# Kernel optimization log

Measured on AMD Instinct MI355X. Metric: run time of the kernel, lower is better.

## Reference

```python
import jax, jax.numpy as jnp
import numpy as np

H = 12
D_MODEL = 768
H_D = D_MODEL // H


def setup_inputs() -> dict:
    key = jax.random.key(0)
    ks = jax.random.split(key, 11)
    B, S = 2, 2048
    scale_in = 1.0
    w_scale = 1.0 / np.sqrt(D_MODEL)
    inp = {
        "query": jax.random.normal(ks[0], (B, S, D_MODEL), dtype=jnp.float32),
        "key": jax.random.normal(ks[1], (B, S, D_MODEL), dtype=jnp.float32),
        "value": jax.random.normal(ks[2], (B, S, D_MODEL), dtype=jnp.float32),
        "wq": jax.random.normal(ks[3], (D_MODEL, D_MODEL), dtype=jnp.float32) * w_scale,
        "bq": jnp.zeros((D_MODEL,), dtype=jnp.float32),
        "wk": jax.random.normal(ks[4], (D_MODEL, D_MODEL), dtype=jnp.float32) * w_scale,
        "bk": jnp.zeros((D_MODEL,), dtype=jnp.float32),
        "wv": jax.random.normal(ks[5], (D_MODEL, D_MODEL), dtype=jnp.float32) * w_scale,
        "bv": jnp.zeros((D_MODEL,), dtype=jnp.float32),
        "wo": jax.random.normal(ks[6], (D_MODEL, D_MODEL), dtype=jnp.float32) * w_scale,
        "bo": jnp.zeros((D_MODEL,), dtype=jnp.float32),
    }
    return inp


def reference(query, key, value, wq, bq, wk, bk, wv, bv, wo, bo):
    B, S, _ = query.shape
    # QKV projections, split into heads: [B, H, S, h_d]
    def proj(x, w, b):
        y = jnp.einsum("bsd,de->bse", x, w) + b
        return y.reshape(B, S, H, H_D).transpose(0, 2, 1, 3)

    q = proj(query, wq, bq)
    k = proj(key, wk, bk)
    v = proj(value, wv, bv)

    # scaled dot-product attention (dropout disabled / eval mode)
    scores = jnp.einsum("bhsd,bhtd->bhst", q, k) / jnp.sqrt(jnp.float32(H_D))
    wm = jax.nn.softmax(scores, axis=-1)  # [B, H, S, S]
    out = jnp.einsum("bhst,bhtd->bhsd", wm, v)

    # merge heads and output projection
    out = out.transpose(0, 2, 1, 3).reshape(B, S, D_MODEL)
    out = jnp.einsum("bsd,de->bse", out, wo) + bo
    return out
```

## Files before the change

kernel.cpp:

```cpp
#include <hip/hip_runtime.h>

#define H 12
#define DM 768
#define HD 64
#define SEQ 2048
#define BATCH 2
#define MROWS (BATCH*SEQ)

typedef __attribute__((ext_vector_type(8))) short short8;
typedef __attribute__((ext_vector_type(4))) float f32x4;
using u16 = unsigned short;
using u32 = unsigned int;

__device__ __forceinline__ float bf2f(u16 u) { return __uint_as_float(((u32)u) << 16); }
__device__ __forceinline__ u16 f2bf(float x) {
  u32 u = __float_as_uint(x);
  return (u16)((u + 0x7fffu + ((u >> 16) & 1u)) >> 16);
}
__device__ __forceinline__ u32 cvt_pk_bf16(float lo, float hi) {
  u32 r;
  asm("v_cvt_pk_bf16_f32 %0, %1, %2" : "=v"(r) : "v"(lo), "v"(hi));
  return r;
}
__device__ __forceinline__ void gl2lds16(const u16* __restrict__ g, u16* l) {
  __builtin_amdgcn_global_load_lds(
      (const __attribute__((address_space(1))) unsigned int*)g,
      (__attribute__((address_space(3))) unsigned int*)l,
      16, 0, 0);
}

#define C_SM 0.18033688011112042f

__global__ __launch_bounds__(256) void transpose_w4(const float* __restrict__ w0, const float* __restrict__ w1,
                                                    const float* __restrict__ w2, const float* __restrict__ w3,
                                                    u16* __restrict__ dst0)
{
  __shared__ u16 Ts[64][72];
  const float* src = blockIdx.z == 0 ? w0 : blockIdx.z == 1 ? w1 : blockIdx.z == 2 ? w2 : w3;
  u16* dst = dst0 + (size_t)blockIdx.z * DM * DM;
  const int t = threadIdx.x;
  const int r0 = blockIdx.y * 64, c0 = blockIdx.x * 64;
  const int row = t >> 2, cq = (t & 3) * 16;
  const float* sp = src + (size_t)(r0 + row) * DM + c0 + cq;
  #pragma unroll
  for (int g = 0; g < 4; ++g) {
    float4 a = *reinterpret_cast<const float4*>(sp + g * 4);
    Ts[row][cq + g * 4 + 0] = f2bf(a.x);
    Ts[row][cq + g * 4 + 1] = f2bf(a.y);
    Ts[row][cq + g * 4 + 2] = f2bf(a.z);
    Ts[row][cq + g * 4 + 3] = f2bf(a.w);
  }
  __syncthreads();
  union { uint4 v[2]; u16 e[16]; } pk;
  #pragma unroll
  for (int j = 0; j < 16; ++j) pk.e[j] = Ts[cq + j][row];
  uint4* dp = reinterpret_cast<uint4*>(dst + (size_t)(c0 + row) * DM + r0 + cq);
  dp[0] = pk.v[0];
  dp[1] = pk.v[1];
}

template<int BM, bool AF32>
__device__ __forceinline__ void gemm_core(const void* __restrict__ Av, const u16* __restrict__ Bt,
                                          const float* __restrict__ bias, void* __restrict__ dstv,
                                          int mode, int bx, int by, float outScale)
{
  constexpr int AFR = BM / 32;
  constexpr int ACH = BM / 32;
  __shared__ u16 As[BM * 64];
  __shared__ u16 Bs[128 * 64];
  const int t = threadIdx.x;
  const int lane = t & 63, w = t >> 6;
  const int l15 = lane & 15, l4 = lane >> 4;
  const int m0 = by * BM, n0 = bx * 128;
  const int wr = (w >> 1) * (BM / 2), wc = (w & 1) * 64;

  f32x4 acc[AFR][4] = {};

  for (int kt = 0; kt < DM / 64; ++kt) {
    const int k0 = kt * 64;
    #pragma unroll
    for (int c = 0; c < ACH; ++c) {
      const int id = c * 256 + t;
      const int row = id >> 3, xc = id & 7;
      const int db = row * 128 + ((xc * 16) ^ ((row & 7) << 4));
      if (AF32) {
        const float* Af = reinterpret_cast<const float*>(Av) + (size_t)(m0 + row) * DM + k0 + xc * 8;
        float4 a0 = *reinterpret_cast<const float4*>(Af);
        float4 a1 = *reinterpret_cast<const float4*>(Af + 4);
        uint4 v;
        v.x = cvt_pk_bf16(a0.x, a0.y);
        v.y = cvt_pk_bf16(a0.z, a0.w);
        v.z = cvt_pk_bf16(a1.x, a1.y);
        v.w = cvt_pk_bf16(a1.z, a1.w);
        *reinterpret_cast<uint4*>(reinterpret_cast<char*>(As) + db) = v;
      } else {
        uint4 va = *reinterpret_cast<const uint4*>(reinterpret_cast<const u16*>(Av) +
                   (size_t)(m0 + row) * DM + k0 + xc * 8);
        *reinterpret_cast<uint4*>(reinterpret_cast<char*>(As) + db) = va;
      }
    }
    #pragma unroll
    for (int c = 0; c < 4; ++c) {
      const int id = c * 256 + t;
      const int row = id >> 3, xc = id & 7;
      const int db = row * 128 + ((xc * 16) ^ ((row & 7) << 4));
      uint4 vb = *reinterpret_cast<const uint4*>(Bt + (size_t)(n0 + row) * DM + k0 + xc * 8);
      *reinterpret_cast<uint4*>(reinterpret_cast<char*>(Bs) + db) = vb;
    }
    __syncthreads();
    #pragma unroll
    for (int ks = 0; ks < 2; ++ks) {
      short8 ag[AFR], bg[4];
      #pragma unroll
      for (int i = 0; i < AFR; ++i) {
        const int ar = wr + i * 16 + l15;
        ag[i] = *reinterpret_cast<const short8*>(reinterpret_cast<const char*>(As) +
                 ar * 128 + ((ks * 64 + l4 * 16) ^ ((ar & 7) << 4)));
      }
      #pragma unroll
      for (int j = 0; j < 4; ++j) {
        const int br = wc + j * 16 + l15;
        bg[j] = *reinterpret_cast<const short8*>(reinterpret_cast<const char*>(Bs) +
                 br * 128 + ((ks * 64 + l4 * 16) ^ ((br & 7) << 4)));
      }
      #pragma unroll
      for (int i = 0; i < AFR; ++i)
        #pragma unroll
        for (int j = 0; j < 4; ++j)
          acc[i][j] = __builtin_amdgcn_mfma_f32_16x16x32_bf16(ag[i], bg[j], acc[i][j], 0, 0, 0);
    }
    __syncthreads();
  }

  #pragma unroll
  for (int j = 0; j < 4; ++j) {
    const int gcol = n0 + wc + j * 16 + l15;
    const float bb = bias[gcol];
    #pragma unroll
    for (int i = 0; i < AFR; ++i) {
      const int grow = m0 + wr + i * 16 + l4 * 4;
      if (mode == 2) {
        float* dst = reinterpret_cast<float*>(dstv);
        #pragma unroll
        for (int r = 0; r < 4; ++r)
          dst[(size_t)(grow + r) * DM + gcol] = acc[i][j][r] + bb;
      } else {
        u16* dst = reinterpret_cast<u16*>(dstv);
        const int b = grow >> 11, s = grow & (SEQ - 1);
        const int h = gcol >> 6, d = gcol & 63;
        if (mode == 0) {
          #pragma unroll
          for (int r = 0; r < 4; ++r)
            dst[((size_t)(b * H + h) * SEQ + s + r) * HD + d] = f2bf((acc[i][j][r] + bb) * outScale);
        } else {
          union { uint2 v; u16 e[4]; } pk;
          #pragma unroll
          for (int r = 0; r < 4; ++r) pk.e[r] = f2bf(acc[i][j][r] + bb);
          *reinterpret_cast<uint2*>(dst + ((size_t)(b * H + h) * HD + d) * SEQ + s) = pk.v;
        }
      }
    }
  }
}

__global__ __launch_bounds__(256) void gemm_qkv_kernel(
    const float* __restrict__ xq, const float* __restrict__ xk, const float* __restrict__ xv,
    const u16* __restrict__ wT, const float* __restrict__ bq, const float* __restrict__ bk,
    const float* __restrict__ bv, u16* __restrict__ Qb, u16* __restrict__ Kb, u16* __restrict__ Vtb)
{
  const int flat = blockIdx.z * 384 + blockIdx.y * 6 + blockIdx.x;
  const int nb = (flat & 7) * 144 + (flat >> 3);
  const int z = nb / 384, rem = nb % 384;
  const int by = rem / 6, bx = rem % 6;
  const float* A    = z == 0 ? xq : z == 1 ? xk : xv;
  const u16* Bt     = wT + (size_t)z * DM * DM;
  const float* bias = z == 0 ? bq : z == 1 ? bk : bv;
  u16* dst          = z == 0 ? Qb : z == 1 ? Kb : Vtb;
  const float sc    = z == 1 ? C_SM : 1.0f;
  gemm_core<64, true>(A, Bt, bias, dst, z == 2 ? 1 : 0, bx, by, sc);
}

__global__ __launch_bounds__(256) void gemm_o_kernel(const u16* __restrict__ A, const u16* __restrict__ woT,
                                                     const float* __restrict__ bo, float* __restrict__ out)
{
  const int flat = blockIdx.y * 6 + blockIdx.x;
  const int nb = (flat & 7) * 96 + (flat >> 3);
  gemm_core<32, false>(A, woT, bo, out, 2, nb % 6, nb / 6, 1.0f);
}

__global__ __launch_bounds__(256) void attn_kernel(const u16* __restrict__ Q, const u16* __restrict__ K,
                                                   const u16* __restrict__ Vt, u16* __restrict__ attn)
{
  __shared__ u16 Ks[2][64 * 64];
  __shared__ u16 Vs[2][64 * 64];
  __shared__ u16 Ps[4][16 * 64];
  const int t = threadIdx.x;
  const int lane = t & 63, w = t >> 6;
  const int l15 = lane & 15, l4 = lane >> 4;
  const int flat = blockIdx.y * 32 + blockIdx.x;
  const int nbid = (flat & 7) * 96 + (flat >> 3);
  const int q0 = (nbid & 31) * 64;
  const int bh = nbid >> 5;
  const size_t qbase  = ((size_t)bh * SEQ + q0) * HD;
  const size_t kbase0 = (size_t)bh * SEQ * HD;
  const size_t vtbase = (size_t)bh * HD * SEQ;

  const int srow = lane >> 3;
  const int scol = ((lane & 7) ^ srow) * 8;

  u16* Qstage = &Ps[0][0];
  #pragma unroll
  for (int j = 0; j < 2; ++j) {
    const int ci = w * 2 + j;
    gl2lds16(Q + qbase + (size_t)(ci * 8 + srow) * HD + scol, &Qstage[ci * 512]);
  }
  #pragma unroll
  for (int j = 0; j < 2; ++j) {
    const int ci = w * 2 + j;
    const int row = ci * 8 + srow;
    gl2lds16(K + kbase0 + (size_t)row * HD + scol, &Ks[0][ci * 512]);
    gl2lds16(Vt + vtbase + (size_t)row * SEQ + scol, &Vs[0][ci * 512]);
  }
  asm volatile("s_waitcnt vmcnt(4)" ::: "memory");
  __builtin_amdgcn_s_barrier();

  short8 qf[2];
  {
    const int qr = w * 16 + l15;
    #pragma unroll
    for (int ks = 0; ks < 2; ++ks)
      qf[ks] = *reinterpret_cast<const short8*>(reinterpret_cast<const char*>(Qstage) +
               qr * 128 + ((ks * 64 + l4 * 16) ^ ((qr & 7) << 4)));
  }
  asm volatile("s_waitcnt lgkmcnt(0)" ::: "memory");
  __builtin_amdgcn_s_barrier();

  short8 ones;
  #pragma unroll
  for (int j = 0; j < 8; ++j) ones[j] = (short)0x3F80;

  f32x4 oacc[4] = {};
  f32x4 accL = {};
  char* Pw = reinterpret_cast<char*>(Ps[w]);
  const int pswz = (l15 & 7) << 4;
  int cur = 0;

  for (int kt = 0; kt < SEQ / 64; ++kt) {
    asm volatile("s_waitcnt vmcnt(0)" ::: "memory");
    __builtin_amdgcn_s_barrier();

    if (kt + 1 < SEQ / 64) {
      const int nxt = cur ^ 1;
      #pragma unroll
      for (int j = 0; j < 2; ++j) {
        const int ci = w * 2 + j;
        const int row = ci * 8 + srow;
        gl2lds16(K + kbase0 + (size_t)((kt + 1) * 64 + row) * HD + scol, &Ks[nxt][ci * 512]);
        gl2lds16(Vt + vtbase + (size_t)row * SEQ + (kt + 1) * 64 + scol, &Vs[nxt][ci * 512]);
      }
    }

    f32x4 sacc[4] = {};
    #pragma unroll
    for (int ks = 0; ks < 2; ++ks) {
      #pragma unroll
      for (int kb = 0; kb < 4; ++kb) {
        const int krow = kb * 16 + l15;
        short8 kf = *reinterpret_cast<const short8*>(reinterpret_cast<const char*>(Ks[cur]) +
                    krow * 128 + ((ks * 64 + l4 * 16) ^ ((krow & 7) << 4)));
        sacc[kb] = __builtin_amdgcn_mfma_f32_16x16x32_bf16(kf, qf[ks], sacc[kb], 0, 0, 0);
      }
    }

    #pragma unroll
    for (int kb = 0; kb < 4; ++kb) {
      const float p0 = exp2f(sacc[kb][0]);
      const float p1 = exp2f(sacc[kb][1]);
      const float p2 = exp2f(sacc[kb][2]);
      const float p3 = exp2f(sacc[kb][3]);
      uint2 pk;
      pk.x = cvt_pk_bf16(p0, p1);
      pk.y = cvt_pk_bf16(p2, p3);
      *reinterpret_cast<uint2*>(Pw + (l15 * 128 + ((kb * 32 + l4 * 8) ^ pswz))) = pk;
    }

    #pragma unroll
    for (int ks = 0; ks < 2; ++ks) {
      short8 pf = *reinterpret_cast<const short8*>(Pw +
                  (l15 * 128 + ((ks * 64 + l4 * 16) ^ pswz)));
      accL = __builtin_amdgcn_mfma_f32_16x16x32_bf16(pf, ones, accL, 0, 0, 0);
      #pragma unroll
      for (int nb = 0; nb < 4; ++nb) {
        const int vrow = nb * 16 + l15;
        short8 vf = *reinterpret_cast<const short8*>(reinterpret_cast<const char*>(Vs[cur]) +
                    vrow * 128 + ((ks * 64 + l4 * 16) ^ ((vrow & 7) << 4)));
        oacc[nb] = __builtin_amdgcn_mfma_f32_16x16x32_bf16(pf, vf, oacc[nb], 0, 0, 0);
      }
    }
    cur ^= 1;
  }

  const int b = bh / H, h = bh % H;
  #pragma unroll
  for (int r = 0; r < 4; ++r) {
    const float inv = 1.f / accL[r];
    const int srow2 = q0 + w * 16 + l4 * 4 + r;
    const size_t base = ((size_t)(b * SEQ + srow2)) * DM + h * HD;
    #pragma unroll
    for (int nb = 0; nb < 4; ++nb)
      attn[base + nb * 16 + l15] = f2bf(oacc[nb][r] * inv);
  }
}

extern "C" void kernel_launch(void* const* d_in, const int* in_sizes, int n_in,
                              void* d_out, int out_size, void* d_ws, size_t ws_size,
                              hipStream_t stream)
{
  const float* q  = (const float*)d_in[0];
  const float* k  = (const float*)d_in[1];
  const float* v  = (const float*)d_in[2];
  const float* wq = (const float*)d_in[3];
  const float* bq = (const float*)d_in[4];
  const float* wk = (const float*)d_in[5];
  const float* bk = (const float*)d_in[6];
  const float* wv = (const float*)d_in[7];
  const float* bv = (const float*)d_in[8];
  const float* wo = (const float*)d_in[9];
  const float* bo = (const float*)d_in[10];

  u16* ws = (u16*)d_ws;
  const size_t WSZ = (size_t)DM * DM;
  const size_t TSZ = (size_t)MROWS * DM;
  u16* wT  = ws;
  u16* Qb  = ws + 4 * WSZ;
  u16* Kb  = Qb + TSZ;
  u16* Vtb = Kb + TSZ;
  u16* Ab  = Vtb + TSZ;

  transpose_w4<<<dim3(12, 12, 4), 256, 0, stream>>>(wq, wk, wv, wo, wT);
  gemm_qkv_kernel<<<dim3(6, 64, 3), 256, 0, stream>>>(q, k, v, wT, bq, bk, bv, Qb, Kb, Vtb);
  attn_kernel<<<dim3(SEQ / 64, BATCH * H), 256, 0, stream>>>(Qb, Kb, Vtb, Ab);
  gemm_o_kernel<<<dim3(6, 128), 256, 0, stream>>>(Ab, wT + 3 * WSZ, bo, (float*)d_out);
}
```

Measured before the change: 108.8 us.

## Rework attention around 32x32 MFMA with register-resident P and 128-query tiles

The attention kernel moves from 16x16x32 to 32x32x16 bf16 MFMA, and each block now handles 128 query rows instead of 64, so every K/V tile loaded into LDS is reused twice as much. P is no longer written to and re-read from LDS. It stays in registers and is redistributed with v_permlane32_swap, and the row sum is computed with scalar adds plus a cross-half shuffle instead of an MFMA against a ones vector. The MFMA sections are wrapped in s_setprio. The trade-offs are higher register pressure and half as many blocks (384), which may lower occupancy and load balance.

```diff
diff --git a/kernel.cpp b/kernel.cpp
--- a/kernel.cpp
+++ b/kernel.cpp
@@ -9,6 +9,7 @@
 
 typedef __attribute__((ext_vector_type(8))) short short8;
 typedef __attribute__((ext_vector_type(4))) float f32x4;
+typedef __attribute__((ext_vector_type(16))) float f32x16;
 using u16 = unsigned short;
 using u32 = unsigned int;
 
@@ -193,56 +194,46 @@
 {
   __shared__ u16 Ks[2][64 * 64];
   __shared__ u16 Vs[2][64 * 64];
-  __shared__ u16 Ps[4][16 * 64];
+  __shared__ u16 Qs[128 * 64];
   const int t = threadIdx.x;
   const int lane = t & 63, w = t >> 6;
-  const int l15 = lane & 15, l4 = lane >> 4;
-  const int flat = blockIdx.y * 32 + blockIdx.x;
-  const int nbid = (flat & 7) * 96 + (flat >> 3);
-  const int q0 = (nbid & 31) * 64;
-  const int bh = nbid >> 5;
+  const int l31 = lane & 31, hi = lane >> 5;
+  const int flat = blockIdx.y * 16 + blockIdx.x;
+  const int nbid = (flat & 7) * 48 + (flat >> 3);
+  const int q0 = (nbid & 15) * 128;
+  const int bh = nbid >> 4;
   const size_t qbase  = ((size_t)bh * SEQ + q0) * HD;
   const size_t kbase0 = (size_t)bh * SEQ * HD;
   const size_t vtbase = (size_t)bh * HD * SEQ;
 
-  const int srow = lane >> 3;
-  const int scol = ((lane & 7) ^ srow) * 8;
-
-  u16* Qstage = &Ps[0][0];
+  const int r8 = lane >> 3;
+  const int pcol = ((lane & 7) ^ r8) * 8;
+
+  #pragma unroll
+  for (int j = 0; j < 4; ++j) {
+    const int ci = w * 4 + j;
+    gl2lds16(Q + qbase + (size_t)(ci * 8 + r8) * HD + pcol, &Qs[ci * 512]);
+  }
   #pragma unroll
   for (int j = 0; j < 2; ++j) {
     const int ci = w * 2 + j;
-    gl2lds16(Q + qbase + (size_t)(ci * 8 + srow) * HD + scol, &Qstage[ci * 512]);
-  }
-  #pragma unroll
-  for (int j = 0; j < 2; ++j) {
-    const int ci = w * 2 + j;
-    const int row = ci * 8 + srow;
-    gl2lds16(K + kbase0 + (size_t)row * HD + scol, &Ks[0][ci * 512]);
-    gl2lds16(Vt + vtbase + (size_t)row * SEQ + scol, &Vs[0][ci * 512]);
+    const int row = ci * 8 + r8;
+    gl2lds16(K + kbase0 + (size_t)row * HD + pcol, &Ks[0][ci * 512]);
+    gl2lds16(Vt + vtbase + (size_t)row * SEQ + pcol, &Vs[0][ci * 512]);
   }
   asm volatile("s_waitcnt vmcnt(4)" ::: "memory");
-  __builtin_amdgcn_s_barrier();
-
-  short8 qf[2];
+
+  short8 qf[4];
   {
-    const int qr = w * 16 + l15;
-    #pragma unroll
-    for (int ks = 0; ks < 2; ++ks)
-      qf[ks] = *reinterpret_cast<const short8*>(reinterpret_cast<const char*>(Qstage) +
-               qr * 128 + ((ks * 64 + l4 * 16) ^ ((qr & 7) << 4)));
-  }
-  asm volatile("s_waitcnt lgkmcnt(0)" ::: "memory");
-  __builtin_amdgcn_s_barrier();
-
-  short8 ones;
-  #pragma unroll
-  for (int j = 0; j < 8; ++j) ones[j] = (short)0x3F80;
-
-  f32x4 oacc[4] = {};
-  f32x4 accL = {};
-  char* Pw = reinterpret_cast<char*>(Ps[w]);
-  const int pswz = (l15 & 7) << 4;
+    const int qr = w * 32 + l31;
+    #pragma unroll
+    for (int ks = 0; ks < 4; ++ks)
+      qf[ks] = *reinterpret_cast<const short8*>(reinterpret_cast<const char*>(Qs) +
+               qr * 128 + (((ks * 32 + hi * 16)) ^ ((qr & 7) << 4)));
+  }
+
+  f32x16 oacc[2] = {};
+  float l_s = 0.f;
   int cur = 0;
 
   for (int kt = 0; kt < SEQ / 64; ++kt) {
@@ -254,61 +245,71 @@
       #pragma unroll
       for (int j = 0; j < 2; ++j) {
         const int ci = w * 2 + j;
-        const int row = ci * 8 + srow;
-        gl2lds16(K + kbase0 + (size_t)((kt + 1) * 64 + row) * HD + scol, &Ks[nxt][ci * 512]);
-        gl2lds16(Vt + vtbase + (size_t)row * SEQ + (kt + 1) * 64 + scol, &Vs[nxt][ci * 512]);
-      }
-    }
-
-    f32x4 sacc[4] = {};
-    #pragma unroll
-    for (int ks = 0; ks < 2; ++ks) {
-      #pragma unroll
-      for (int kb = 0; kb < 4; ++kb) {
-        const int krow = kb * 16 + l15;
-        short8 kf = *reinterpret_cast<const short8*>(reinterpret_cast<const char*>(Ks[cur]) +
-                    krow * 128 + ((ks * 64 + l4 * 16) ^ ((krow & 7) << 4)));
-        sacc[kb] = __builtin_amdgcn_mfma_f32_16x16x32_bf16(kf, qf[ks], sacc[kb], 0, 0, 0);
-      }
-    }
-
-    #pragma unroll
-    for (int kb = 0; kb < 4; ++kb) {
-      const float p0 = exp2f(sacc[kb][0]);
-      const float p1 = exp2f(sacc[kb][1]);
-      const float p2 = exp2f(sacc[kb][2]);
-      const float p3 = exp2f(sacc[kb][3]);
-      uint2 pk;
-      pk.x = cvt_pk_bf16(p0, p1);
-      pk.y = cvt_pk_bf16(p2, p3);
-      *reinterpret_cast<uint2*>(Pw + (l15 * 128 + ((kb * 32 + l4 * 8) ^ pswz))) = pk;
-    }
-
-    #pragma unroll
-    for (int ks = 0; ks < 2; ++ks) {
-      short8 pf = *reinterpret_cast<const short8*>(Pw +
-                  (l15 * 128 + ((ks * 64 + l4 * 16) ^ pswz)));
-      accL = __builtin_amdgcn_mfma_f32_16x16x32_bf16(pf, ones, accL, 0, 0, 0);
-      #pragma unroll
-      for (int nb = 0; nb < 4; ++nb) {
-        const int vrow = nb * 16 + l15;
+        const int row = ci * 8 + r8;
+        gl2lds16(K + kbase0 + (size_t)((kt + 1) * 64 + row) * HD + pcol, &Ks[nxt][ci * 512]);
+        gl2lds16(Vt + vtbase + (size_t)row * SEQ + (kt + 1) * 64 + pcol, &Vs[nxt][ci * 512]);
+      }
+    }
+
+    f32x16 s0 = {}, s1 = {};
+    __builtin_amdgcn_s_setprio(1);
+    #pragma unroll
+    for (int ks = 0; ks < 4; ++ks) {
+      const int cb = ks * 32 + hi * 16;
+      short8 kf0 = *reinterpret_cast<const short8*>(reinterpret_cast<const char*>(Ks[cur]) +
+                   l31 * 128 + (cb ^ ((l31 & 7) << 4)));
+      short8 kf1 = *reinterpret_cast<const short8*>(reinterpret_cast<const char*>(Ks[cur]) +
+                   (32 + l31) * 128 + (cb ^ ((l31 & 7) << 4)));
+      s0 = __builtin_amdgcn_mfma_f32_32x32x16_bf16(kf0, qf[ks], s0, 0, 0, 0);
+      s1 = __builtin_amdgcn_mfma_f32_32x32x16_bf16(kf1, qf[ks], s1, 0, 0, 0);
+    }
+    __builtin_amdgcn_s_setprio(0);
+
+    float p0[16], p1[16], psum = 0.f;
+    #pragma unroll
+    for (int r = 0; r < 16; ++r) {
+      p0[r] = exp2f(s0[r]);
+      p1[r] = exp2f(s1[r]);
+      psum += p0[r] + p1[r];
+    }
+    l_s += psum;
+
+    __builtin_amdgcn_s_setprio(1);
+    #pragma unroll
+    for (int ks2 = 0; ks2 < 4; ++ks2) {
+      const float* P = (ks2 < 2) ? p0 : p1;
+      const int ro = (ks2 & 1) * 8;
+      u32 a0 = cvt_pk_bf16(P[ro + 0], P[ro + 1]);
+      u32 a1 = cvt_pk_bf16(P[ro + 2], P[ro + 3]);
+      u32 b0 = cvt_pk_bf16(P[ro + 4], P[ro + 5]);
+      u32 b1 = cvt_pk_bf16(P[ro + 6], P[ro + 7]);
+      asm volatile("v_permlane32_swap_b32 %0, %1" : "+v"(a0), "+v"(b0));
+      asm volatile("v_permlane32_swap_b32 %0, %1" : "+v"(a1), "+v"(b1));
+      union { u32 u[4]; short8 s; } pa;
+      pa.u[0] = a0; pa.u[1] = a1; pa.u[2] = b0; pa.u[3] = b1;
+      const int cb2 = ks2 * 32 + hi * 16;
+      #pragma unroll
+      for (int dt = 0; dt < 2; ++dt) {
+        const int vr = dt * 32 + l31;
         short8 vf = *reinterpret_cast<const short8*>(reinterpret_cast<const char*>(Vs[cur]) +
-                    vrow * 128 + ((ks * 64 + l4 * 16) ^ ((vrow & 7) << 4)));
-        oacc[nb] = __builtin_amdgcn_mfma_f32_16x16x32_bf16(pf, vf, oacc[nb], 0, 0, 0);
-      }
-    }
+                    vr * 128 + (cb2 ^ ((vr & 7) << 4)));
+        oacc[dt] = __builtin_amdgcn_mfma_f32_32x32x16_bf16(pa.s, vf, oacc[dt], 0, 0, 0);
+      }
+    }
+    __builtin_amdgcn_s_setprio(0);
     cur ^= 1;
   }
 
+  const float l_tot = l_s + __shfl_xor(l_s, 32);
   const int b = bh / H, h = bh % H;
   #pragma unroll
-  for (int r = 0; r < 4; ++r) {
-    const float inv = 1.f / accL[r];
-    const int srow2 = q0 + w * 16 + l4 * 4 + r;
-    const size_t base = ((size_t)(b * SEQ + srow2)) * DM + h * HD;
-    #pragma unroll
-    for (int nb = 0; nb < 4; ++nb)
-      attn[base + nb * 16 + l15] = f2bf(oacc[nb][r] * inv);
+  for (int r = 0; r < 16; ++r) {
+    const int qo = (r & 3) + 8 * (r >> 2) + 4 * hi;
+    const float inv = 1.f / __shfl(l_tot, qo);
+    const int qg = q0 + w * 32 + qo;
+    const size_t base = ((size_t)(b * SEQ + qg)) * DM + h * HD;
+    attn[base + l31]      = f2bf(oacc[0][r] * inv);
+    attn[base + 32 + l31] = f2bf(oacc[1][r] * inv);
   }
 }
 
@@ -339,6 +340,6 @@
 
   transpose_w4<<<dim3(12, 12, 4), 256, 0, stream>>>(wq, wk, wv, wo, wT);
   gemm_qkv_kernel<<<dim3(6, 64, 3), 256, 0, stream>>>(q, k, v, wT, bq, bk, bv, Qb, Kb, Vtb);
-  attn_kernel<<<dim3(SEQ / 64, BATCH * H), 256, 0, stream>>>(Qb, Kb, Vtb, Ab);
+  attn_kernel<<<dim3(16, BATCH * H), 256, 0, stream>>>(Qb, Kb, Vtb, Ab);
   gemm_o_kernel<<<dim3(6, 128), 256, 0, stream>>>(Ab, wT + 3 * WSZ, bo, (float*)d_out);
 }
```

After: 116.5 us. 1.07x slower.
